# Performance work log

Measured on AMD Instinct MI355X. Metric: run time of the kernel, lower is better.

Reference implementation:

```python
import jax, jax.numpy as jnp
import numpy as np

N_NODES = 100000
N_EDGES = 1000000
HIDDEN = 64
IN_DIM = 4


def setup_inputs() -> dict:
    key = jax.random.key(0)
    ks = jax.random.split(key, 7)
    x = jax.random.normal(ks[0], (N_NODES, IN_DIM), dtype=jnp.float32)
    edges = jax.random.randint(ks[1], (N_EDGES, 2), 0, N_NODES, dtype=jnp.int32)
    W1 = jax.random.normal(ks[2], (IN_DIM, HIDDEN), dtype=jnp.float32) * 0.5
    b1 = jax.random.normal(ks[3], (HIDDEN,), dtype=jnp.float32) * 0.1
    phases = jax.random.normal(ks[4], (N_EDGES,), dtype=jnp.float32) * 0.1
    Wout = jax.random.normal(ks[5], (HIDDEN, 1), dtype=jnp.float32) * 0.1
    bout = jax.random.normal(ks[6], (1,), dtype=jnp.float32) * 0.1
    return {"x": x, "edges": edges, "W1": W1, "b1": b1,
            "phases": phases, "Wout": Wout, "bout": bout}


def reference(x, edges, W1, b1, phases, Wout, bout):
    # h = lin(x): [N, D]
    h = x @ W1 + b1
    u = edges[:, 0]  # [E]
    v = edges[:, 1]  # [E]
    c = jnp.cos(phases)  # [E]
    s = jnp.sin(phases)  # [E]
    hu = h[u]  # [E, D] gather
    hv = h[v]  # [E, D] gather
    # rot only mixes the first two channels; the rest pass through (eye).
    # msg to v: rot @ h[u] -> [c*h0 - s*h1, s*h0 + c*h1, h2, ...]
    msg_v = jnp.concatenate([
        (c * hu[:, 0] - s * hu[:, 1])[:, None],
        (s * hu[:, 0] + c * hu[:, 1])[:, None],
        hu[:, 2:],
    ], axis=1)
    # msg to u: rot.T @ h[v] -> [c*h0 + s*h1, -s*h0 + c*h1, h2, ...]
    msg_u = jnp.concatenate([
        (c * hv[:, 0] + s * hv[:, 1])[:, None],
        (-s * hv[:, 0] + c * hv[:, 1])[:, None],
        hv[:, 2:],
    ], axis=1)
    diffused = jnp.zeros_like(h).at[v].add(msg_v).at[u].add(msg_u)  # scatter-add
    return (h + diffused) @ Wout + bout  # [N, 1]
```

## Files before the change

kernel.cpp:

```cpp
#include <hip/hip_runtime.h>
#include <hip/hip_fp16.h>

#define N_NODES 100000
#define N_EDGES 1000000
#define HIDDEN 64

#define N_RANGES 3
#define C_RANGE 33344
#define N_SLICES 85
#define PAIRS (N_EDGES / 2)
#define PPB ((PAIRS + N_SLICES - 1) / N_SLICES)
#define A_THREADS 1024
#define E_THREADS 512

__device__ __forceinline__ void compute_consts(
    const float* __restrict__ W1, const float* __restrict__ b1,
    const float* __restrict__ Wout, const float* __restrict__ bout,
    float* kc, int tid) {
    if (tid < 64) {
        float wj = Wout[tid];
        float p0 = W1[0 * HIDDEN + tid] * wj;
        float p1 = W1[1 * HIDDEN + tid] * wj;
        float p2 = W1[2 * HIDDEN + tid] * wj;
        float p3 = W1[3 * HIDDEN + tid] * wj;
        float pb = b1[tid] * wj;
        #pragma unroll
        for (int off = 32; off > 0; off >>= 1) {
            p0 += __shfl_down(p0, off);
            p1 += __shfl_down(p1, off);
            p2 += __shfl_down(p2, off);
            p3 += __shfl_down(p3, off);
            pb += __shfl_down(pb, off);
        }
        if (tid < 4) {
            kc[5 + tid] = W1[tid * HIDDEN + 0];
            kc[9 + tid] = W1[tid * HIDDEN + 1];
        }
        if (tid == 0) {
            kc[0] = p0; kc[1] = p1; kc[2] = p2; kc[3] = p3; kc[4] = pb;
            kc[13] = b1[0]; kc[14] = b1[1];
            kc[15] = Wout[0]; kc[16] = Wout[1];
            kc[17] = bout[0];
        }
    }
}

__device__ __forceinline__ float contrib(
    float4 xe, float cs, float sn_signed,
    float c0, float c1, float c2, float c3, float cb,
    float a0, float a1, float a2, float a3,
    float g0, float g1, float g2, float g3,
    float b10, float b11, float w0, float w1) {
    float h0 = xe.x * a0 + xe.y * a1 + xe.z * a2 + xe.w * a3 + b10;
    float h1 = xe.x * g0 + xe.y * g1 + xe.z * g2 + xe.w * g3 + b11;
    float d  = xe.x * c0 + xe.y * c1 + xe.z * c2 + xe.w * c3 + cb;
    float a  = h0 * w0 + h1 * w1;
    float b  = h0 * w1 - h1 * w0;
    return cs * a + sn_signed * b + (d - a);
}

__device__ __forceinline__ unsigned pack_half2(float x, float y) {
    __half2 h = __floats2half2_rn(x, y);
    return *(unsigned*)&h;
}

__global__ __launch_bounds__(E_THREADS) void edge_kernel(
    const int4* __restrict__ epairs, const float2* __restrict__ ppairs,
    const float4* __restrict__ x4,
    const float* __restrict__ W1, const float* __restrict__ b1,
    const float* __restrict__ Wout, const float* __restrict__ bout,
    uint2* __restrict__ t4) {
    __shared__ float kc[18];
    compute_consts(W1, b1, Wout, bout, kc, threadIdx.x);
    __syncthreads();
    int p = blockIdx.x * E_THREADS + threadIdx.x;
    if (p >= PAIRS) return;

    const float c0 = kc[0], c1 = kc[1], c2 = kc[2], c3 = kc[3], cb = kc[4];
    const float a0 = kc[5], a1 = kc[6], a2 = kc[7], a3 = kc[8];
    const float g0 = kc[9], g1 = kc[10], g2 = kc[11], g3 = kc[12];
    const float b10 = kc[13], b11 = kc[14], w0 = kc[15], w1 = kc[16];

    int4   ee = epairs[p];
    float2 pp = ppairs[p];

    float4 xu0 = x4[ee.x];
    float4 xv0 = x4[ee.y];
    float4 xu1 = x4[ee.z];
    float4 xv1 = x4[ee.w];

    float sn0, cs0, sn1, cs1;
    __sincosf(pp.x, &sn0, &cs0);
    __sincosf(pp.y, &sn1, &cs1);

    float tv0 = contrib(xu0, cs0,  sn0, c0,c1,c2,c3,cb, a0,a1,a2,a3, g0,g1,g2,g3, b10,b11,w0,w1);
    float tu0 = contrib(xv0, cs0, -sn0, c0,c1,c2,c3,cb, a0,a1,a2,a3, g0,g1,g2,g3, b10,b11,w0,w1);
    float tv1 = contrib(xu1, cs1,  sn1, c0,c1,c2,c3,cb, a0,a1,a2,a3, g0,g1,g2,g3, b10,b11,w0,w1);
    float tu1 = contrib(xv1, cs1, -sn1, c0,c1,c2,c3,cb, a0,a1,a2,a3, g0,g1,g2,g3, b10,b11,w0,w1);

    t4[p] = make_uint2(pack_half2(tv0, tu0), pack_half2(tv1, tu1));
}

__global__ __launch_bounds__(A_THREADS) void bin_kernel(
    const int4* __restrict__ epairs, const uint2* __restrict__ t4,
    __half* __restrict__ part) {
    __shared__ __align__(16) float bins[C_RANGE];
    const int tid = threadIdx.x;
    const int r = blockIdx.x / N_SLICES;
    const int s = blockIdx.x - r * N_SLICES;

    {
        float4 z = make_float4(0.f, 0.f, 0.f, 0.f);
        float4* b4 = (float4*)bins;
        for (int j = tid; j < C_RANGE / 4; j += A_THREADS) b4[j] = z;
    }
    __syncthreads();

    const int nlo = r * C_RANGE;
    const int pA = s * PPB;
    const int pB = min(pA + PPB, PAIRS);

    #pragma unroll 2
    for (int p = pA + tid; p < pB; p += A_THREADS) {
        int4  ee = epairs[p];
        uint2 tt = t4[p];

        float2 t01 = __half22float2(*(const __half2*)&tt.x);
        float2 t23 = __half22float2(*(const __half2*)&tt.y);

        unsigned jv0 = (unsigned)(ee.y - nlo);
        unsigned ju0 = (unsigned)(ee.x - nlo);
        unsigned jv1 = (unsigned)(ee.w - nlo);
        unsigned ju1 = (unsigned)(ee.z - nlo);

        if (jv0 < C_RANGE) atomicAdd(&bins[jv0], t01.x);
        if (ju0 < C_RANGE) atomicAdd(&bins[ju0], t01.y);
        if (jv1 < C_RANGE) atomicAdd(&bins[jv1], t23.x);
        if (ju1 < C_RANGE) atomicAdd(&bins[ju1], t23.y);
    }
    __syncthreads();

    uint2* __restrict__ d2 = (uint2*)(part + (size_t)blockIdx.x * C_RANGE);
    const float4* b4 = (const float4*)bins;
    for (int j = tid; j < C_RANGE / 4; j += A_THREADS) {
        float4 v = b4[j];
        d2[j] = make_uint2(pack_half2(v.x, v.y), pack_half2(v.z, v.w));
    }
}

__global__ __launch_bounds__(512) void reduce_kernel(
    const float4* __restrict__ x4,
    const float* __restrict__ W1, const float* __restrict__ b1,
    const float* __restrict__ Wout, const float* __restrict__ bout,
    const __half2* __restrict__ part2, float2* __restrict__ out2) {
    __shared__ float kc[18];
    compute_consts(W1, b1, Wout, bout, kc, threadIdx.x);
    __syncthreads();
    int t = blockIdx.x * 512 + threadIdx.x;
    int i0 = t * 2;
    if (i0 >= N_NODES) return;
    int r = i0 / C_RANGE;
    int j = i0 - r * C_RANGE;
    const __half2* __restrict__ p = part2
        + (size_t)(r * N_SLICES) * (C_RANGE / 2) + (j >> 1);
    float s0 = 0.0f, s1 = 0.0f;
    #pragma unroll 5
    for (int s = 0; s < N_SLICES; s++) {
        float2 v = __half22float2(p[(size_t)s * (C_RANGE / 2)]);
        s0 += v.x; s1 += v.y;
    }
    float4 xa = x4[i0];
    float4 xb = x4[i0 + 1];
    float base = kc[4] + kc[17];
    out2[t] = make_float2(
        s0 + xa.x * kc[0] + xa.y * kc[1] + xa.z * kc[2] + xa.w * kc[3] + base,
        s1 + xb.x * kc[0] + xb.y * kc[1] + xb.z * kc[2] + xb.w * kc[3] + base);
}

__global__ void precompute_kernel(const float* __restrict__ W1,
                                  const float* __restrict__ b1,
                                  const float* __restrict__ Wout,
                                  const float* __restrict__ bout,
                                  float* __restrict__ consts) {
    __shared__ float kc[18];
    compute_consts(W1, b1, Wout, bout, kc, threadIdx.x);
    __syncthreads();
    if (threadIdx.x < 18) consts[threadIdx.x] = kc[threadIdx.x];
}

__global__ void edge_atomic_kernel(const int2* __restrict__ edges,
                                   const float* __restrict__ phases,
                                   const float4* __restrict__ x4,
                                   const float* __restrict__ consts,
                                   float* __restrict__ rep) {
    int e = blockIdx.x * blockDim.x + threadIdx.x;
    if (e >= N_EDGES) return;
    float c0 = consts[0], c1 = consts[1], c2 = consts[2], c3 = consts[3];
    float cb = consts[4];
    float a0 = consts[5], a1 = consts[6], a2 = consts[7], a3 = consts[8];
    float g0 = consts[9], g1 = consts[10], g2 = consts[11], g3 = consts[12];
    float b10 = consts[13], b11 = consts[14], w0 = consts[15], w1 = consts[16];
    int2 ed = edges[e];
    float ph = phases[e];
    float sn, cs;
    __sincosf(ph, &sn, &cs);
    float4 xu = x4[ed.x];
    float4 xv = x4[ed.y];
    atomicAdd(rep + ed.y, contrib(xu, cs,  sn, c0,c1,c2,c3,cb, a0,a1,a2,a3, g0,g1,g2,g3, b10,b11,w0,w1));
    atomicAdd(rep + ed.x, contrib(xv, cs, -sn, c0,c1,c2,c3,cb, a0,a1,a2,a3, g0,g1,g2,g3, b10,b11,w0,w1));
}

__global__ void final_kernel(const float4* __restrict__ x4,
                             const float* __restrict__ consts,
                             const float* __restrict__ rep,
                             float* __restrict__ out) {
    int i = blockIdx.x * blockDim.x + threadIdx.x;
    if (i >= N_NODES) return;
    float4 xi = x4[i];
    out[i] = rep[i] + xi.x * consts[0] + xi.y * consts[1] + xi.z * consts[2]
           + xi.w * consts[3] + consts[4] + consts[17];
}

extern "C" void kernel_launch(void* const* d_in, const int* in_sizes, int n_in,
                              void* d_out, int out_size, void* d_ws, size_t ws_size,
                              hipStream_t stream) {
    const float* x      = (const float*)d_in[0];
    const int*   edges  = (const int*)d_in[1];
    const float* W1     = (const float*)d_in[2];
    const float* b1     = (const float*)d_in[3];
    const float* phases = (const float*)d_in[4];
    const float* Wout   = (const float*)d_in[5];
    const float* bout   = (const float*)d_in[6];
    float* out = (float*)d_out;

    const size_t part_bytes =
        (size_t)N_RANGES * N_SLICES * C_RANGE * sizeof(__half);
    const size_t t4_off   = part_bytes;
    const size_t t4_bytes = (size_t)PAIRS * sizeof(uint2);
    const size_t need     = t4_off + t4_bytes;

    if (ws_size >= need) {
        __half* part = (__half*)d_ws;
        uint2*  t4   = (uint2*)((char*)d_ws + t4_off);
        edge_kernel<<<(PAIRS + E_THREADS - 1) / E_THREADS, E_THREADS, 0, stream>>>(
            (const int4*)edges, (const float2*)phases, (const float4*)x,
            W1, b1, Wout, bout, t4);
        bin_kernel<<<N_RANGES * N_SLICES, A_THREADS, 0, stream>>>(
            (const int4*)edges, t4, part);
        reduce_kernel<<<(N_NODES / 2 + 511) / 512, 512, 0, stream>>>(
            (const float4*)x, W1, b1, Wout, bout,
            (const __half2*)part, (float2*)out);
    } else {
        float* consts = (float*)d_ws;
        float* rep    = (float*)((char*)d_ws + 256);
        hipMemsetAsync(rep, 0, N_NODES * sizeof(float), stream);
        precompute_kernel<<<1, 64, 0, stream>>>(W1, b1, Wout, bout, consts);
        edge_atomic_kernel<<<(N_EDGES + 255) / 256, 256, 0, stream>>>(
            (const int2*)edges, phases, (const float4*)x, consts, rep);
        final_kernel<<<(N_NODES + 255) / 256, 256, 0, stream>>>(
            (const float4*)x, consts, rep, out);
    }
}
```

Before: 109.6 us.

## Bucket edge contributions by node range before shared-memory binning

The edge kernel now computes per-edge contributions and writes them, with local node offsets, into per-range buckets using wave ballots and LDS counters. The bin kernel reads only entries for its range instead of scanning all edges and filtering. This removes the threefold redundant reading of edges and contribution data. In exchange it adds ballot and atomic partitioning overhead, larger fp32 bucket writes, and a fixed per-segment capacity that could overflow on skewed inputs.

```diff
diff --git a/kernel.cpp b/kernel.cpp
--- a/kernel.cpp
+++ b/kernel.cpp
@@ -9,9 +9,12 @@
 #define C_RANGE 33344
 #define N_SLICES 85
 #define PAIRS (N_EDGES / 2)
-#define PPB ((PAIRS + N_SLICES - 1) / N_SLICES)
 #define A_THREADS 1024
-#define E_THREADS 512
+
+#define NSEG_P 255
+#define P_THREADS 1024
+#define PPB_P ((PAIRS + NSEG_P - 1) / NSEG_P)
+#define SEG_CAP 7936
 
 __device__ __forceinline__ void compute_consts(
     const float* __restrict__ W1, const float* __restrict__ b1,
@@ -64,45 +67,83 @@
     return *(unsigned*)&h;
 }
 
-__global__ __launch_bounds__(E_THREADS) void edge_kernel(
+__global__ __launch_bounds__(P_THREADS) void partition_kernel(
     const int4* __restrict__ epairs, const float2* __restrict__ ppairs,
     const float4* __restrict__ x4,
     const float* __restrict__ W1, const float* __restrict__ b1,
     const float* __restrict__ Wout, const float* __restrict__ bout,
-    uint2* __restrict__ t4) {
+    uint2* __restrict__ bucket, unsigned* __restrict__ counts) {
     __shared__ float kc[18];
-    compute_consts(W1, b1, Wout, bout, kc, threadIdx.x);
-    __syncthreads();
-    int p = blockIdx.x * E_THREADS + threadIdx.x;
-    if (p >= PAIRS) return;
+    __shared__ unsigned blk_cnt[N_RANGES];
+    const int tid = threadIdx.x;
+    const int lane = tid & 63;
+
+    compute_consts(W1, b1, Wout, bout, kc, tid);
+    if (tid < N_RANGES) blk_cnt[tid] = 0;
+    __syncthreads();
 
     const float c0 = kc[0], c1 = kc[1], c2 = kc[2], c3 = kc[3], cb = kc[4];
     const float a0 = kc[5], a1 = kc[6], a2 = kc[7], a3 = kc[8];
     const float g0 = kc[9], g1 = kc[10], g2 = kc[11], g3 = kc[12];
     const float b10 = kc[13], b11 = kc[14], w0 = kc[15], w1 = kc[16];
 
-    int4   ee = epairs[p];
-    float2 pp = ppairs[p];
-
-    float4 xu0 = x4[ee.x];
-    float4 xv0 = x4[ee.y];
-    float4 xu1 = x4[ee.z];
-    float4 xv1 = x4[ee.w];
-
-    float sn0, cs0, sn1, cs1;
-    __sincosf(pp.x, &sn0, &cs0);
-    __sincosf(pp.y, &sn1, &cs1);
-
-    float tv0 = contrib(xu0, cs0,  sn0, c0,c1,c2,c3,cb, a0,a1,a2,a3, g0,g1,g2,g3, b10,b11,w0,w1);
-    float tu0 = contrib(xv0, cs0, -sn0, c0,c1,c2,c3,cb, a0,a1,a2,a3, g0,g1,g2,g3, b10,b11,w0,w1);
-    float tv1 = contrib(xu1, cs1,  sn1, c0,c1,c2,c3,cb, a0,a1,a2,a3, g0,g1,g2,g3, b10,b11,w0,w1);
-    float tu1 = contrib(xv1, cs1, -sn1, c0,c1,c2,c3,cb, a0,a1,a2,a3, g0,g1,g2,g3, b10,b11,w0,w1);
-
-    t4[p] = make_uint2(pack_half2(tv0, tu0), pack_half2(tv1, tu1));
+    const int pA = blockIdx.x * PPB_P;
+    const int pB = min(pA + PPB_P, PAIRS);
+
+    auto scatter = [&](int dest, float t, bool valid) {
+        unsigned rr = valid ? ((unsigned)dest) / (unsigned)C_RANGE : 3u;
+        unsigned lo = (unsigned)dest - rr * (unsigned)C_RANGE;
+        #pragma unroll
+        for (unsigned r = 0; r < N_RANGES; ++r) {
+            unsigned long long mask = __ballot(rr == r);
+            if (mask) {
+                int leader = __ffsll((long long)mask) - 1;
+                unsigned base = 0;
+                if (lane == leader)
+                    base = atomicAdd(&blk_cnt[r], (unsigned)__popcll(mask));
+                base = __shfl(base, leader);
+                if (rr == r) {
+                    unsigned ofs = (unsigned)__popcll(mask & ((1ull << lane) - 1));
+                    bucket[(size_t)(r * NSEG_P + blockIdx.x) * SEG_CAP + base + ofs]
+                        = make_uint2(lo, __float_as_uint(t));
+                }
+            }
+        }
+    };
+
+    #pragma unroll
+    for (int k = 0; k < (PPB_P + P_THREADS - 1) / P_THREADS; ++k) {
+        int p = pA + tid + k * P_THREADS;
+        bool valid = p < pB;
+        int pc = valid ? p : 0;
+        int4   ee = epairs[pc];
+        float2 pp = ppairs[pc];
+
+        float4 xu0 = x4[ee.x];
+        float4 xv0 = x4[ee.y];
+        float4 xu1 = x4[ee.z];
+        float4 xv1 = x4[ee.w];
+
+        float sn0, cs0, sn1, cs1;
+        __sincosf(pp.x, &sn0, &cs0);
+        __sincosf(pp.y, &sn1, &cs1);
+
+        float tv0 = contrib(xu0, cs0,  sn0, c0,c1,c2,c3,cb, a0,a1,a2,a3, g0,g1,g2,g3, b10,b11,w0,w1);
+        float tu0 = contrib(xv0, cs0, -sn0, c0,c1,c2,c3,cb, a0,a1,a2,a3, g0,g1,g2,g3, b10,b11,w0,w1);
+        float tv1 = contrib(xu1, cs1,  sn1, c0,c1,c2,c3,cb, a0,a1,a2,a3, g0,g1,g2,g3, b10,b11,w0,w1);
+        float tu1 = contrib(xv1, cs1, -sn1, c0,c1,c2,c3,cb, a0,a1,a2,a3, g0,g1,g2,g3, b10,b11,w0,w1);
+
+        scatter(ee.y, tv0, valid);
+        scatter(ee.x, tu0, valid);
+        scatter(ee.w, tv1, valid);
+        scatter(ee.z, tu1, valid);
+    }
+    __syncthreads();
+    if (tid < N_RANGES) counts[tid * NSEG_P + blockIdx.x] = blk_cnt[tid];
 }
 
 __global__ __launch_bounds__(A_THREADS) void bin_kernel(
-    const int4* __restrict__ epairs, const uint2* __restrict__ t4,
+    const uint2* __restrict__ bucket, const unsigned* __restrict__ counts,
     __half* __restrict__ part) {
     __shared__ __align__(16) float bins[C_RANGE];
     const int tid = threadIdx.x;
@@ -116,27 +157,13 @@
     }
     __syncthreads();
 
-    const int nlo = r * C_RANGE;
-    const int pA = s * PPB;
-    const int pB = min(pA + PPB, PAIRS);
-
-    #pragma unroll 2
-    for (int p = pA + tid; p < pB; p += A_THREADS) {
-        int4  ee = epairs[p];
-        uint2 tt = t4[p];
-
-        float2 t01 = __half22float2(*(const __half2*)&tt.x);
-        float2 t23 = __half22float2(*(const __half2*)&tt.y);
-
-        unsigned jv0 = (unsigned)(ee.y - nlo);
-        unsigned ju0 = (unsigned)(ee.x - nlo);
-        unsigned jv1 = (unsigned)(ee.w - nlo);
-        unsigned ju1 = (unsigned)(ee.z - nlo);
-
-        if (jv0 < C_RANGE) atomicAdd(&bins[jv0], t01.x);
-        if (ju0 < C_RANGE) atomicAdd(&bins[ju0], t01.y);
-        if (jv1 < C_RANGE) atomicAdd(&bins[jv1], t23.x);
-        if (ju1 < C_RANGE) atomicAdd(&bins[ju1], t23.y);
+    for (int seg = s; seg < NSEG_P; seg += N_SLICES) {
+        unsigned cnt = counts[r * NSEG_P + seg];
+        const uint2* __restrict__ e = bucket + (size_t)(r * NSEG_P + seg) * SEG_CAP;
+        for (unsigned j = tid; j < cnt; j += A_THREADS) {
+            uint2 v = e[j];
+            atomicAdd(&bins[v.x], __uint_as_float(v.y));
+        }
     }
     __syncthreads();
 
@@ -235,18 +262,22 @@
 
     const size_t part_bytes =
         (size_t)N_RANGES * N_SLICES * C_RANGE * sizeof(__half);
-    const size_t t4_off   = part_bytes;
-    const size_t t4_bytes = (size_t)PAIRS * sizeof(uint2);
-    const size_t need     = t4_off + t4_bytes;
+    const size_t bucket_off   = part_bytes;
+    const size_t bucket_bytes =
+        (size_t)N_RANGES * NSEG_P * SEG_CAP * sizeof(uint2);
+    const size_t counts_off   = bucket_off + bucket_bytes;
+    const size_t counts_bytes = (size_t)N_RANGES * NSEG_P * sizeof(unsigned);
+    const size_t need         = counts_off + counts_bytes;
 
     if (ws_size >= need) {
-        __half* part = (__half*)d_ws;
-        uint2*  t4   = (uint2*)((char*)d_ws + t4_off);
-        edge_kernel<<<(PAIRS + E_THREADS - 1) / E_THREADS, E_THREADS, 0, stream>>>(
+        __half*   part   = (__half*)d_ws;
+        uint2*    bucket = (uint2*)((char*)d_ws + bucket_off);
+        unsigned* counts = (unsigned*)((char*)d_ws + counts_off);
+        partition_kernel<<<NSEG_P, P_THREADS, 0, stream>>>(
             (const int4*)edges, (const float2*)phases, (const float4*)x,
-            W1, b1, Wout, bout, t4);
+            W1, b1, Wout, bout, bucket, counts);
         bin_kernel<<<N_RANGES * N_SLICES, A_THREADS, 0, stream>>>(
-            (const int4*)edges, t4, part);
+            bucket, counts, part);
         reduce_kernel<<<(N_NODES / 2 + 511) / 512, 512, 0, stream>>>(
             (const float4*)x, W1, b1, Wout, bout,
             (const __half2*)part, (float2*)out);
```

Measured after the change: 113.4 us. 3.4% more time.
